# Kernel optimization log

Measured on AMD Instinct MI355X. Metric: run time of the kernel, lower is better.

The kernel has to match this reference:

```python
import jax, jax.numpy as jnp
import numpy as np
import math

NUM_HEADS = 16
HIDDEN = 1024
HEAD = HIDDEN // NUM_HEADS


def setup_inputs() -> dict:
    key = jax.random.key(0)
    ks = jax.random.split(key, 11)
    B, S, H = 2, 2048, HIDDEN
    s = 1.0 / math.sqrt(H)
    return {
        "q": jax.random.normal(ks[0], (B, S, H), jnp.float32),
        "k": jax.random.normal(ks[1], (B, S, H), jnp.float32),
        "v": jax.random.normal(ks[2], (B, S, H), jnp.float32),
        "Wq": jax.random.normal(ks[3], (H, H), jnp.float32) * s,
        "bq": jnp.zeros((H,), jnp.float32),
        "Wk": jax.random.normal(ks[4], (H, H), jnp.float32) * s,
        "bk": jnp.zeros((H,), jnp.float32),
        "Wv": jax.random.normal(ks[5], (H, H), jnp.float32) * s,
        "bv": jnp.zeros((H,), jnp.float32),
        "Wo": jax.random.normal(ks[6], (H, H), jnp.float32) * s,
        "bo": jnp.zeros((H,), jnp.float32),
    }


def reference(q, k, v, Wq, bq, Wk, bk, Wv, bv, Wo, bo):
    B, S, H = q.shape
    nh, hd = NUM_HEADS, HEAD
    # projections (torch Linear: x @ W.T + b)
    qp = (q @ Wq.T + bq).reshape(B, S, nh, hd).transpose(0, 2, 1, 3)  # [B,nh,S,hd]
    kp = (k @ Wk.T + bk).reshape(B, S, nh, hd).transpose(0, 2, 1, 3)
    vp = (v @ Wv.T + bv).reshape(B, S, nh, hd).transpose(0, 2, 1, 3)
    scores = jnp.einsum('bhqd,bhkd->bhqk', qp, kp) / math.sqrt(hd)
    attn = jax.nn.softmax(scores, axis=-1)  # [B,nh,S,S]
    o = jnp.einsum('bhqk,bhkd->bhqd', attn, vp)
    o = o.transpose(0, 2, 1, 3).reshape(B, S, H)
    return o @ Wo.T + bo
```

## Files before the change

kernel.cpp:

```cpp
#include <hip/hip_runtime.h>
#include <cstdint>
#include <type_traits>
#include <utility>

typedef __attribute__((ext_vector_type(8))) short short8;
typedef __attribute__((ext_vector_type(8))) _Float16 f16x8_t;
typedef __attribute__((ext_vector_type(4))) float f32x4;

template <typename V, typename = void>
struct mfma_h_takes : std::false_type {};
template <typename V>
struct mfma_h_takes<V, std::void_t<decltype(__builtin_amdgcn_mfma_f32_16x16x32_f16(
    std::declval<V>(), std::declval<V>(), std::declval<f32x4>(), 0, 0, 0))>>
    : std::true_type {};

using hfrag_t = std::conditional_t<mfma_h_takes<f16x8_t>::value, f16x8_t, short8>;
static_assert(mfma_h_takes<f16x8_t>::value || mfma_h_takes<short8>::value,
              "no usable mfma_f32_16x16x32_f16 signature");

__device__ __forceinline__ f32x4 mfma16h(hfrag_t a, hfrag_t b, f32x4 c) {
  return __builtin_amdgcn_mfma_f32_16x16x32_f16(a, b, c, 0, 0, 0);
}

__device__ __forceinline__ void gld_lds16(const void* g, void* l) {
  __builtin_amdgcn_global_load_lds(
      (const __attribute__((address_space(1))) void*)(uintptr_t)g,
      (__attribute__((address_space(3))) void*)(uint32_t)(uintptr_t)l, 16, 0, 0);
}

__device__ __forceinline__ uint16_t f16_rne(float x) {
  return __builtin_bit_cast(uint16_t, (_Float16)x);
}
__device__ __forceinline__ float f16_up(uint16_t h) {
  return (float)__builtin_bit_cast(_Float16, h);
}

__device__ __forceinline__ float exp2_fast(float x) {
#if __has_builtin(__builtin_amdgcn_exp2f)
  return __builtin_amdgcn_exp2f(x);
#else
  return exp2f(x);
#endif
}
__device__ __forceinline__ uint32_t pk_f16(float a, float b) {
#if __has_builtin(__builtin_amdgcn_cvt_pkrtz)
  return __builtin_bit_cast(uint32_t, __builtin_amdgcn_cvt_pkrtz(a, b));
#else
  union { uint16_t u[2]; uint32_t w; } r;
  r.u[0] = f16_rne(a);
  r.u[1] = f16_rne(b);
  return r.w;
#endif
}

__device__ __forceinline__ int swz(int row, int col) {
  return row * 64 + ((((col >> 3) + row) & 7) << 3) + (col & 7);
}

struct SplitArgs {
  const float* src[4];
  uint16_t* hi[4];
  uint16_t* lo[4];
  int n4;
};
__global__ void split_multi(SplitArgs a) {
  const int z = blockIdx.y;
  int i = blockIdx.x * 256 + threadIdx.x;
  if (i >= a.n4) return;
  float4 x = ((const float4*)a.src[z])[i];
  ushort4 h;
  h.x = f16_rne(x.x);
  h.y = f16_rne(x.y);
  h.z = f16_rne(x.z);
  h.w = f16_rne(x.w);
  ((ushort4*)a.hi[z])[i] = h;
  if (a.lo[z]) {
    ushort4 l;
    l.x = f16_rne(x.x - f16_up(h.x));
    l.y = f16_rne(x.y - f16_up(h.y));
    l.z = f16_rne(x.z - f16_up(h.z));
    l.w = f16_rne(x.w - f16_up(h.w));
    ((ushort4*)a.lo[z])[i] = l;
  }
}

struct QKVArgs {
  const uint16_t* Ah[3];
  const uint16_t* Bh[3];
  const float* bias[3];
  uint16_t* oH[3];
  uint16_t* oL[3];
};

__global__ __launch_bounds__(256, 3) void gemm_qkv(QKVArgs args) {
  __shared__ uint16_t lds[2][128][64];
  const int K = 1024;
  const int tid = threadIdx.x;
  const int wv = tid >> 6, lane = tid & 63;
  const int lm = lane & 15, g = lane >> 4;
  const int wm = (wv & 1) * 64, wn = (wv >> 1) * 64;
  const int z = blockIdx.z;
  const bool isT = (z == 2);
  const int t = blockIdx.x + 8 * blockIdx.y;
  const int kx = t & 7, j = t >> 3;
  const int sx = (j & 3) | ((kx & 1) << 2);
  const int sy = (j >> 2) | ((kx >> 1) << 3);
  const int gm0 = (isT ? sx : sy) * 128;
  const int gn0 = (isT ? sy : sx) * 128;

  const uint16_t* base[2] = {args.Ah[z] + (size_t)gm0 * K,
                             args.Bh[z] + (size_t)gn0 * K};
  const int rl8 = lane >> 3;
  const int scl = (((lane & 7) - rl8) & 7) * 8;

  f32x4 acc[4][4];
#pragma unroll
  for (int a = 0; a < 4; ++a)
#pragma unroll
    for (int b = 0; b < 4; ++b) acc[a][b] = (f32x4)0.0f;

#pragma unroll 1
  for (int kt = 0; kt < K; kt += 64) {
#pragma unroll
    for (int jj = 0; jj < 8; ++jj) {
      const int c = wv + 4 * jj;
      const int p = c >> 4, r8 = (c & 15) * 8;
      gld_lds16(base[p] + (size_t)(r8 + rl8) * K + kt + scl, &lds[p][r8][0]);
    }
    __syncthreads();
#pragma unroll
    for (int ks = 0; ks < 2; ++ks) {
      const int uc = ((ks * 4 + g + lm) & 7) * 8;
      hfrag_t af[4];
#pragma unroll
      for (int mf = 0; mf < 4; ++mf) {
        af[mf] = *(const hfrag_t*)&lds[0][wm + mf * 16 + lm][uc];
      }
#pragma unroll
      for (int nf = 0; nf < 4; ++nf) {
        hfrag_t bhf = *(const hfrag_t*)&lds[1][wn + nf * 16 + lm][uc];
#pragma unroll
        for (int mf = 0; mf < 4; ++mf) {
          acc[mf][nf] = mfma16h(af[mf], bhf, acc[mf][nf]);
        }
      }
    }
    __syncthreads();
  }
  const float* bias = args.bias[z];
  uint16_t* oH = args.oH[z];
  uint16_t* oL = args.oL[z];
#pragma unroll
  for (int mf = 0; mf < 4; ++mf) {
#pragma unroll
    for (int nf = 0; nf < 4; ++nf) {
      const int col = gn0 + wn + nf * 16 + lm;
#pragma unroll
      for (int i = 0; i < 4; ++i) {
        const int row = gm0 + wm + mf * 16 + g * 4 + i;
        float v = acc[mf][nf][i] + (isT ? bias[row] : bias[col]);
        uint16_t h = f16_rne(v);
        size_t addr;
        if (!isT) {
          addr = ((size_t)((row >> 11) * 16 + (col >> 6)) * 2048 + (row & 2047)) * 64 +
                 (col & 63);
        } else {
          addr = ((size_t)((col >> 11) * 1024 + row)) * 2048 + (col & 2047);
        }
        oH[addr] = h;
        if (oL) oL[addr] = f16_rne(v - f16_up(h));
      }
    }
  }
}

__global__ __launch_bounds__(256, 2) void gemm_o(
    const uint16_t* __restrict__ Ah, const uint16_t* __restrict__ Bh,
    const float* __restrict__ bias, float* __restrict__ out) {
  const int K = 1024, N = 1024;
  __shared__ uint16_t ldsA[64][64];
  __shared__ uint16_t ldsB[128][64];
  const int tid = threadIdx.x;
  const int wv = tid >> 6, lane = tid & 63;
  const int lm = lane & 15, g = lane >> 4;
  const int wm = (wv & 1) * 32, wn = (wv >> 1) * 64;
  const int t = blockIdx.x + 8 * blockIdx.y;
  const int kx = t & 7, j = t >> 3;
  const int sx = (j & 3) | ((kx & 1) << 2);
  const int sy = (j >> 2) | ((kx >> 1) << 4);
  const int gm0 = sy * 64, gn0 = sx * 128;
  const uint16_t* baseA = Ah + (size_t)gm0 * K;
  const uint16_t* baseB = Bh + (size_t)gn0 * K;
  const int rl8 = lane >> 3;
  const int scl = (((lane & 7) - rl8) & 7) * 8;

  f32x4 acc[2][4];
#pragma unroll
  for (int a = 0; a < 2; ++a)
#pragma unroll
    for (int b = 0; b < 4; ++b) acc[a][b] = (f32x4)0.0f;

#pragma unroll 1
  for (int kt = 0; kt < K; kt += 64) {
#pragma unroll
    for (int jj = 0; jj < 6; ++jj) {
      const int c = wv + 4 * jj;
      if (c < 8) {
        gld_lds16(baseA + (size_t)(c * 8 + rl8) * K + kt + scl, &ldsA[c * 8][0]);
      } else {
        const int b = c - 8;
        gld_lds16(baseB + (size_t)(b * 8 + rl8) * K + kt + scl, &ldsB[b * 8][0]);
      }
    }
    __syncthreads();
#pragma unroll
    for (int ks = 0; ks < 2; ++ks) {
      const int uc = ((ks * 4 + g + lm) & 7) * 8;
      hfrag_t af[2];
#pragma unroll
      for (int mf = 0; mf < 2; ++mf) {
        af[mf] = *(const hfrag_t*)&ldsA[wm + mf * 16 + lm][uc];
      }
#pragma unroll
      for (int nf = 0; nf < 4; ++nf) {
        hfrag_t bhf = *(const hfrag_t*)&ldsB[wn + nf * 16 + lm][uc];
#pragma unroll
        for (int mf = 0; mf < 2; ++mf) {
          acc[mf][nf] = mfma16h(af[mf], bhf, acc[mf][nf]);
        }
      }
    }
    __syncthreads();
  }
#pragma unroll
  for (int mf = 0; mf < 2; ++mf)
#pragma unroll
    for (int nf = 0; nf < 4; ++nf) {
      const int col = gn0 + wn + nf * 16 + lm;
#pragma unroll
      for (int i = 0; i < 4; ++i) {
        const int row = gm0 + wm + mf * 16 + g * 4 + i;
        out[(size_t)row * N + col] = acc[mf][nf][i] + bias[col];
      }
    }
}

__global__ __launch_bounds__(256, 2) void attn_kernel(
    const uint16_t* __restrict__ Qh,
    const uint16_t* __restrict__ Kh,
    const uint16_t* __restrict__ Vh,
    float* __restrict__ opart, float* __restrict__ lpart) {
  __shared__ uint16_t kt[4096];
  __shared__ uint16_t vt[4096];
  __shared__ uint16_t pp[8192];
  const int tid = threadIdx.x;
  const int wave = tid >> 6, lane = tid & 63;
  const int lm = lane & 15, g = lane >> 4;
  const int linear = blockIdx.x + 32 * blockIdx.y;
  const int bh = (linear & 7) + 8 * (linear >> 8);
  const int qt = (linear >> 3) & 15;
  const int half = (linear >> 7) & 1;
  const int kvh = half * 1024;
  const size_t base = (size_t)bh * 131072;
  const int q0 = qt * 128 + wave * 32;

  hfrag_t qf[2][2];
#pragma unroll
  for (int b = 0; b < 2; ++b) {
    const size_t rb = base + (size_t)(q0 + b * 16 + lm) * 64 + g * 8;
    qf[b][0] = *(const hfrag_t*)(Qh + rb);
    qf[b][1] = *(const hfrag_t*)(Qh + rb + 32);
  }
  f32x4 oacc[2][4];
  f32x4 lacc[2];
#pragma unroll
  for (int mf = 0; mf < 2; ++mf) {
    lacc[mf] = (f32x4)0.0f;
#pragma unroll
    for (int nf = 0; nf < 4; ++nf) oacc[mf][nf] = (f32x4)0.0f;
  }
  short8 ones_s = (short8)(short)0x3C00;
  hfrag_t ones = __builtin_bit_cast(hfrag_t, ones_s);

  const int sr = tid >> 3;
  const int sc = (tid & 7) * 8;

  uint4 kr0, kr1, vr0, vr1;
  {
    const size_t ka = base + (size_t)(kvh + sr) * 64 + sc;
    kr0 = *(const uint4*)(Kh + ka);
    kr1 = *(const uint4*)(Kh + ka + 2048);
  }

  const float kExpScale = 0.12500000f * 1.44269504f;

#pragma unroll 1
  for (int it = 0; it < 16; ++it) {
    const int kv0 = kvh + it * 64;
    *(uint4*)&kt[swz(sr, sc)] = kr0;
    *(uint4*)&kt[swz(sr + 32, sc)] = kr1;
    __syncthreads();
    {
      const size_t va = base + (size_t)sr * 2048 + kv0 + sc;
      vr0 = *(const uint4*)(Vh + va);
      vr1 = *(const uint4*)(Vh + va + 65536);
    }
    f32x4 sct[4][2];
#pragma unroll
    for (int a = 0; a < 4; ++a)
#pragma unroll
      for (int b = 0; b < 2; ++b) sct[a][b] = (f32x4)0.0f;
    __builtin_amdgcn_s_setprio(1);
#pragma unroll
    for (int ks = 0; ks < 2; ++ks) {
#pragma unroll
      for (int a = 0; a < 4; ++a) {
        hfrag_t kfh = *(const hfrag_t*)&kt[swz(a * 16 + lm, ks * 32 + g * 8)];
#pragma unroll
        for (int b = 0; b < 2; ++b) {
          sct[a][b] = mfma16h(kfh, qf[b][ks], sct[a][b]);
        }
      }
    }
    __builtin_amdgcn_s_setprio(0);
#pragma unroll
    for (int a = 0; a < 4; ++a) {
#pragma unroll
      for (int b = 0; b < 2; ++b) {
        float e0 = exp2_fast(fminf(kExpScale * sct[a][b][0], 15.0f));
        float e1 = exp2_fast(fminf(kExpScale * sct[a][b][1], 15.0f));
        float e2 = exp2_fast(fminf(kExpScale * sct[a][b][2], 15.0f));
        float e3 = exp2_fast(fminf(kExpScale * sct[a][b][3], 15.0f));
        uint2 pk;
        pk.x = pk_f16(e0, e1);
        pk.y = pk_f16(e2, e3);
        *(uint2*)&pp[swz(wave * 32 + b * 16 + lm, a * 16 + g * 4)] = pk;
      }
    }
    *(uint4*)&vt[swz(sr, sc)] = vr0;
    *(uint4*)&vt[swz(sr + 32, sc)] = vr1;
    __syncthreads();
    if (it + 1 < 16) {
      const size_t ka = base + (size_t)(kv0 + 64 + sr) * 64 + sc;
      kr0 = *(const uint4*)(Kh + ka);
      kr1 = *(const uint4*)(Kh + ka + 2048);
    }
    __builtin_amdgcn_s_setprio(1);
#pragma unroll
    for (int ks = 0; ks < 2; ++ks) {
      hfrag_t pa[2];
#pragma unroll
      for (int mf = 0; mf < 2; ++mf) {
        pa[mf] = *(const hfrag_t*)&pp[swz(wave * 32 + mf * 16 + lm, ks * 32 + g * 8)];
        lacc[mf] = mfma16h(pa[mf], ones, lacc[mf]);
      }
#pragma unroll
      for (int nf = 0; nf < 4; ++nf) {
        hfrag_t vbh = *(const hfrag_t*)&vt[swz(nf * 16 + lm, ks * 32 + g * 8)];
#pragma unroll
        for (int mf = 0; mf < 2; ++mf) {
          oacc[mf][nf] = mfma16h(pa[mf], vbh, oacc[mf][nf]);
        }
      }
    }
    __builtin_amdgcn_s_setprio(0);
  }
  const int obase = (half * 32 + bh) * 2048;
#pragma unroll
  for (int mf = 0; mf < 2; ++mf) {
#pragma unroll
    for (int i = 0; i < 4; ++i) {
      const int qrow = qt * 128 + wave * 32 + mf * 16 + g * 4 + i;
      float* orow = opart + ((size_t)obase + qrow) * 64;
#pragma unroll
      for (int nf = 0; nf < 4; ++nf) orow[nf * 16 + lm] = oacc[mf][nf][i];
      if (lm == 0) lpart[obase + qrow] = lacc[mf][i];
    }
  }
}

__global__ void combine_kernel(const float* __restrict__ opart,
                               const float* __restrict__ lpart,
                               uint16_t* __restrict__ oh) {
  const int idx = blockIdx.x * 256 + threadIdx.x;
  const float4 a = ((const float4*)opart)[idx];
  const float4 b = ((const float4*)(opart + 4194304))[idx];
  const int row = idx >> 4;
  const float linv = 1.0f / (lpart[row] + lpart[65536 + row]);
  const int bh = row >> 11, qq = row & 2047;
  const int bb = bh >> 4, hh = bh & 15;
  const size_t o = ((size_t)(bb * 2048 + qq)) * 1024 + hh * 64 + (idx & 15) * 4;
  ushort4 H;
  H.x = f16_rne((a.x + b.x) * linv);
  H.y = f16_rne((a.y + b.y) * linv);
  H.z = f16_rne((a.z + b.z) * linv);
  H.w = f16_rne((a.w + b.w) * linv);
  *(ushort4*)(oh + o) = H;
}

extern "C" void kernel_launch(void* const* d_in, const int* in_sizes, int n_in,
                              void* d_out, int out_size, void* d_ws, size_t ws_size,
                              hipStream_t stream) {
  const float* q = (const float*)d_in[0];
  const float* k = (const float*)d_in[1];
  const float* v = (const float*)d_in[2];
  const float* Wq = (const float*)d_in[3];
  const float* bq = (const float*)d_in[4];
  const float* Wk = (const float*)d_in[5];
  const float* bk = (const float*)d_in[6];
  const float* Wv = (const float*)d_in[7];
  const float* bv = (const float*)d_in[8];
  const float* Wo = (const float*)d_in[9];
  const float* bo = (const float*)d_in[10];

  const size_t NX = 4194304;
  const size_t NW = 1048576;
  uint16_t* p = (uint16_t*)d_ws;
  uint16_t* xqh = p; p += NX; uint16_t* xql = p; p += NX;
  uint16_t* xkh = p; p += NX; uint16_t* xkl = p; p += NX;
  uint16_t* xvh = p; p += NX; uint16_t* xvl = p; p += NX;
  uint16_t* wqh = p; p += NW; uint16_t* wql = p; p += NW;
  uint16_t* wkh = p; p += NW; uint16_t* wkl = p; p += NW;
  uint16_t* wvh = p; p += NW; uint16_t* wvl = p; p += NW;
  uint16_t* woh = p; p += NW; uint16_t* wol = p; p += NW;
  uint16_t* qph = p; p += NX; uint16_t* qpl = p; p += NX;
  uint16_t* kph = p; p += NX; uint16_t* kpl = p; p += NX;
  uint16_t* vth = p; p += NX; uint16_t* vtl = p; p += NX;
  uint16_t* oh = xqh;
  float* opart = (float*)xkh;
  float* lpart = opart + 2 * 4194304;

  SplitArgs sx;
  sx.src[0] = q;  sx.hi[0] = xqh; sx.lo[0] = nullptr;
  sx.src[1] = k;  sx.hi[1] = xkh; sx.lo[1] = nullptr;
  sx.src[2] = v;  sx.hi[2] = xvh; sx.lo[2] = nullptr;
  sx.src[3] = nullptr; sx.hi[3] = nullptr; sx.lo[3] = nullptr;
  sx.n4 = (int)(NX / 4);
  split_multi<<<dim3((unsigned)(NX / 4 / 256), 3), 256, 0, stream>>>(sx);

  SplitArgs sw;
  sw.src[0] = Wq; sw.hi[0] = wqh; sw.lo[0] = nullptr;
  sw.src[1] = Wk; sw.hi[1] = wkh; sw.lo[1] = nullptr;
  sw.src[2] = Wv; sw.hi[2] = wvh; sw.lo[2] = nullptr;
  sw.src[3] = Wo; sw.hi[3] = woh; sw.lo[3] = nullptr;
  sw.n4 = (int)(NW / 4);
  split_multi<<<dim3((unsigned)(NW / 4 / 256), 4), 256, 0, stream>>>(sw);

  QKVArgs qa;
  qa.Ah[0] = xqh; qa.Bh[0] = wqh; qa.bias[0] = bq; qa.oH[0] = qph; qa.oL[0] = nullptr;
  qa.Ah[1] = xkh; qa.Bh[1] = wkh; qa.bias[1] = bk; qa.oH[1] = kph; qa.oL[1] = nullptr;
  qa.Ah[2] = wvh; qa.Bh[2] = xvh; qa.bias[2] = bv; qa.oH[2] = vth; qa.oL[2] = nullptr;
  gemm_qkv<<<dim3(8, 32, 3), 256, 0, stream>>>(qa);

  attn_kernel<<<dim3(32, 32), 256, 0, stream>>>(qph, kph, vth, opart, lpart);
  combine_kernel<<<4096, 256, 0, stream>>>(opart, lpart, oh);

  gemm_o<<<dim3(8, 64), 256, 0, stream>>>(oh, woh, bo, (float*)d_out);
}
```

Measured before the change: 237.2 us.

## Double-buffer LDS in projection GEMMs, fold softmax scale into Q, prefetch K earlier

Both projection GEMMs now double-buffer their LDS tiles, issuing the next tile's global-to-LDS loads before computing the current one. They wait on vmcnt with a raw barrier instead of syncing twice per iteration with no prefetch. The softmax scale and log2e factor are folded into the Q projection epilogue, which removes a multiply per score element in the attention loop. The attention kernel also issues the next K-tile loads earlier, overlapping them with the QK^T MFMAs. In exchange, gemm_qkv uses twice the LDS and its occupancy hint drops from 3 to 2 blocks, and Q is rounded to fp16 after scaling.

```diff
diff --git a/kernel.cpp b/kernel.cpp
--- a/kernel.cpp
+++ b/kernel.cpp
@@ -92,8 +92,8 @@
   uint16_t* oL[3];
 };
 
-__global__ __launch_bounds__(256, 3) void gemm_qkv(QKVArgs args) {
-  __shared__ uint16_t lds[2][128][64];
+__global__ __launch_bounds__(256, 2) void gemm_qkv(QKVArgs args) {
+  __shared__ uint16_t lds[2][2][128][64];
   const int K = 1024;
   const int tid = threadIdx.x;
   const int wv = tid >> 6, lane = tid & 63;
@@ -119,37 +119,57 @@
 #pragma unroll
     for (int b = 0; b < 4; ++b) acc[a][b] = (f32x4)0.0f;
 
+#pragma unroll
+  for (int jj = 0; jj < 8; ++jj) {
+    const int c = wv + 4 * jj;
+    const int p = c >> 4, r8 = (c & 15) * 8;
+    gld_lds16(base[p] + (size_t)(r8 + rl8) * K + 0 + scl, &lds[0][p][r8][0]);
+  }
+
 #pragma unroll 1
-  for (int kt = 0; kt < K; kt += 64) {
-#pragma unroll
-    for (int jj = 0; jj < 8; ++jj) {
-      const int c = wv + 4 * jj;
-      const int p = c >> 4, r8 = (c & 15) * 8;
-      gld_lds16(base[p] + (size_t)(r8 + rl8) * K + kt + scl, &lds[p][r8][0]);
-    }
-    __syncthreads();
+  for (int ti = 0; ti < 16; ++ti) {
+    const int cur = ti & 1;
+    if (ti + 1 < 16) {
+      const int kt = (ti + 1) * 64;
+#pragma unroll
+      for (int jj = 0; jj < 8; ++jj) {
+        const int c = wv + 4 * jj;
+        const int p = c >> 4, r8 = (c & 15) * 8;
+        gld_lds16(base[p] + (size_t)(r8 + rl8) * K + kt + scl,
+                  &lds[cur ^ 1][p][r8][0]);
+      }
+      asm volatile("s_waitcnt vmcnt(8)" ::: "memory");
+    } else {
+      asm volatile("s_waitcnt vmcnt(0)" ::: "memory");
+    }
+    __builtin_amdgcn_sched_barrier(0);
+    __builtin_amdgcn_s_barrier();
+    __builtin_amdgcn_sched_barrier(0);
 #pragma unroll
     for (int ks = 0; ks < 2; ++ks) {
       const int uc = ((ks * 4 + g + lm) & 7) * 8;
       hfrag_t af[4];
 #pragma unroll
       for (int mf = 0; mf < 4; ++mf) {
-        af[mf] = *(const hfrag_t*)&lds[0][wm + mf * 16 + lm][uc];
+        af[mf] = *(const hfrag_t*)&lds[cur][0][wm + mf * 16 + lm][uc];
       }
 #pragma unroll
       for (int nf = 0; nf < 4; ++nf) {
-        hfrag_t bhf = *(const hfrag_t*)&lds[1][wn + nf * 16 + lm][uc];
+        hfrag_t bhf = *(const hfrag_t*)&lds[cur][1][wn + nf * 16 + lm][uc];
 #pragma unroll
         for (int mf = 0; mf < 4; ++mf) {
           acc[mf][nf] = mfma16h(af[mf], bhf, acc[mf][nf]);
         }
       }
     }
-    __syncthreads();
+    __builtin_amdgcn_sched_barrier(0);
+    __builtin_amdgcn_s_barrier();
+    __builtin_amdgcn_sched_barrier(0);
   }
   const float* bias = args.bias[z];
   uint16_t* oH = args.oH[z];
   uint16_t* oL = args.oL[z];
+  const float kQScale = 0.18033688f;
 #pragma unroll
   for (int mf = 0; mf < 4; ++mf) {
 #pragma unroll
@@ -159,6 +179,7 @@
       for (int i = 0; i < 4; ++i) {
         const int row = gm0 + wm + mf * 16 + g * 4 + i;
         float v = acc[mf][nf][i] + (isT ? bias[row] : bias[col]);
+        if (z == 0) v *= kQScale;
         uint16_t h = f16_rne(v);
         size_t addr;
         if (!isT) {
@@ -178,8 +199,8 @@
     const uint16_t* __restrict__ Ah, const uint16_t* __restrict__ Bh,
     const float* __restrict__ bias, float* __restrict__ out) {
   const int K = 1024, N = 1024;
-  __shared__ uint16_t ldsA[64][64];
-  __shared__ uint16_t ldsB[128][64];
+  __shared__ uint16_t ldsA[2][64][64];
+  __shared__ uint16_t ldsB[2][128][64];
   const int tid = threadIdx.x;
   const int wv = tid >> 6, lane = tid & 63;
   const int lm = lane & 15, g = lane >> 4;
@@ -200,37 +221,61 @@
 #pragma unroll
     for (int b = 0; b < 4; ++b) acc[a][b] = (f32x4)0.0f;
 
+#pragma unroll
+  for (int jj = 0; jj < 6; ++jj) {
+    const int c = wv + 4 * jj;
+    if (c < 8) {
+      gld_lds16(baseA + (size_t)(c * 8 + rl8) * K + 0 + scl, &ldsA[0][c * 8][0]);
+    } else {
+      const int b = c - 8;
+      gld_lds16(baseB + (size_t)(b * 8 + rl8) * K + 0 + scl, &ldsB[0][b * 8][0]);
+    }
+  }
+
 #pragma unroll 1
-  for (int kt = 0; kt < K; kt += 64) {
-#pragma unroll
-    for (int jj = 0; jj < 6; ++jj) {
-      const int c = wv + 4 * jj;
-      if (c < 8) {
-        gld_lds16(baseA + (size_t)(c * 8 + rl8) * K + kt + scl, &ldsA[c * 8][0]);
-      } else {
-        const int b = c - 8;
-        gld_lds16(baseB + (size_t)(b * 8 + rl8) * K + kt + scl, &ldsB[b * 8][0]);
-      }
-    }
-    __syncthreads();
+  for (int ti = 0; ti < 16; ++ti) {
+    const int cur = ti & 1;
+    if (ti + 1 < 16) {
+      const int kt = (ti + 1) * 64;
+#pragma unroll
+      for (int jj = 0; jj < 6; ++jj) {
+        const int c = wv + 4 * jj;
+        if (c < 8) {
+          gld_lds16(baseA + (size_t)(c * 8 + rl8) * K + kt + scl,
+                    &ldsA[cur ^ 1][c * 8][0]);
+        } else {
+          const int b = c - 8;
+          gld_lds16(baseB + (size_t)(b * 8 + rl8) * K + kt + scl,
+                    &ldsB[cur ^ 1][b * 8][0]);
+        }
+      }
+      asm volatile("s_waitcnt vmcnt(6)" ::: "memory");
+    } else {
+      asm volatile("s_waitcnt vmcnt(0)" ::: "memory");
+    }
+    __builtin_amdgcn_sched_barrier(0);
+    __builtin_amdgcn_s_barrier();
+    __builtin_amdgcn_sched_barrier(0);
 #pragma unroll
     for (int ks = 0; ks < 2; ++ks) {
       const int uc = ((ks * 4 + g + lm) & 7) * 8;
       hfrag_t af[2];
 #pragma unroll
       for (int mf = 0; mf < 2; ++mf) {
-        af[mf] = *(const hfrag_t*)&ldsA[wm + mf * 16 + lm][uc];
+        af[mf] = *(const hfrag_t*)&ldsA[cur][wm + mf * 16 + lm][uc];
       }
 #pragma unroll
       for (int nf = 0; nf < 4; ++nf) {
-        hfrag_t bhf = *(const hfrag_t*)&ldsB[wn + nf * 16 + lm][uc];
+        hfrag_t bhf = *(const hfrag_t*)&ldsB[cur][wn + nf * 16 + lm][uc];
 #pragma unroll
         for (int mf = 0; mf < 2; ++mf) {
           acc[mf][nf] = mfma16h(af[mf], bhf, acc[mf][nf]);
         }
       }
     }
-    __syncthreads();
+    __builtin_amdgcn_sched_barrier(0);
+    __builtin_amdgcn_s_barrier();
+    __builtin_amdgcn_sched_barrier(0);
   }
 #pragma unroll
   for (int mf = 0; mf < 2; ++mf)
@@ -292,8 +337,6 @@
     kr1 = *(const uint4*)(Kh + ka + 2048);
   }
 
-  const float kExpScale = 0.12500000f * 1.44269504f;
-
 #pragma unroll 1
   for (int it = 0; it < 16; ++it) {
     const int kv0 = kvh + it * 64;
@@ -305,6 +348,11 @@
       vr0 = *(const uint4*)(Vh + va);
       vr1 = *(const uint4*)(Vh + va + 65536);
     }
+    if (it + 1 < 16) {
+      const size_t ka = base + (size_t)(kv0 + 64 + sr) * 64 + sc;
+      kr0 = *(const uint4*)(Kh + ka);
+      kr1 = *(const uint4*)(Kh + ka + 2048);
+    }
     f32x4 sct[4][2];
 #pragma unroll
     for (int a = 0; a < 4; ++a)
@@ -327,10 +375,10 @@
     for (int a = 0; a < 4; ++a) {
 #pragma unroll
       for (int b = 0; b < 2; ++b) {
-        float e0 = exp2_fast(fminf(kExpScale * sct[a][b][0], 15.0f));
-        float e1 = exp2_fast(fminf(kExpScale * sct[a][b][1], 15.0f));
-        float e2 = exp2_fast(fminf(kExpScale * sct[a][b][2], 15.0f));
-        float e3 = exp2_fast(fminf(kExpScale * sct[a][b][3], 15.0f));
+        float e0 = exp2_fast(fminf(sct[a][b][0], 15.0f));
+        float e1 = exp2_fast(fminf(sct[a][b][1], 15.0f));
+        float e2 = exp2_fast(fminf(sct[a][b][2], 15.0f));
+        float e3 = exp2_fast(fminf(sct[a][b][3], 15.0f));
         uint2 pk;
         pk.x = pk_f16(e0, e1);
         pk.y = pk_f16(e2, e3);
@@ -340,11 +388,6 @@
     *(uint4*)&vt[swz(sr, sc)] = vr0;
     *(uint4*)&vt[swz(sr + 32, sc)] = vr1;
     __syncthreads();
-    if (it + 1 < 16) {
-      const size_t ka = base + (size_t)(kv0 + 64 + sr) * 64 + sc;
-      kr0 = *(const uint4*)(Kh + ka);
-      kr1 = *(const uint4*)(Kh + ka + 2048);
-    }
     __builtin_amdgcn_s_setprio(1);
 #pragma unroll
     for (int ks = 0; ks < 2; ++ks) {
```

Result: no change. 237.6 us (+0.2%).
